# Performance work log

Measured on AMD Instinct MI355X. Metric: run time of the kernel, lower is better.

## Reference

```python
import jax, jax.numpy as jnp
import numpy as np

DIM = 1024
HEADS = 16


def setup_inputs() -> dict:
    key = jax.random.key(0)
    k1, k2, k3, k4 = jax.random.split(key, 4)
    x = jax.random.normal(k1, (2, 2048, DIM), dtype=jnp.float32)
    # nn.Linear(dim, dim*3, bias=False): weight [3*dim, dim], y = x @ W.T
    w_qkv = jax.random.normal(k2, (3 * DIM, DIM), dtype=jnp.float32) * (DIM ** -0.5)
    # nn.Linear(dim, dim) with bias
    w_out = jax.random.normal(k3, (DIM, DIM), dtype=jnp.float32) * (DIM ** -0.5)
    b_out = jax.random.normal(k4, (DIM,), dtype=jnp.float32) * 0.01
    return {"x": x, "w_qkv": w_qkv, "w_out": w_out, "b_out": b_out}


def reference(x, w_qkv, w_out, b_out):
    B, L, D = x.shape
    H = HEADS
    hd = D // H
    scale = D ** -0.5  # NOTE: module scales by full dim, not head_dim
    qkv = jnp.einsum('bld,ed->ble', x, w_qkv)          # [B, L, 3D]
    qkv = qkv.reshape(B, L, 3, H, hd)
    q = jnp.transpose(qkv[:, :, 0], (0, 2, 1, 3))       # [B, H, L, hd]
    k = jnp.transpose(qkv[:, :, 1], (0, 2, 1, 3))
    v = jnp.transpose(qkv[:, :, 2], (0, 2, 1, 3))
    attn = jnp.einsum('bhqd,bhkd->bhqk', q, k) * scale  # [B, H, L, L]
    attn = jax.nn.softmax(attn, axis=-1)
    o = jnp.einsum('bhqk,bhkd->bhqd', attn, v)           # [B, H, L, hd]
    o = jnp.transpose(o, (0, 2, 1, 3)).reshape(B, L, D)
    return jnp.einsum('bld,ed->ble', o, w_out) + b_out
```

## Files before the change

### kernel.cpp

```cpp
#include <hip/hip_runtime.h>


typedef __bf16 bf16;
typedef __bf16 bf16x4 __attribute__((ext_vector_type(4)));
typedef __bf16 bf16x8 __attribute__((ext_vector_type(8)));
typedef float  f32x4 __attribute__((ext_vector_type(4)));

#define MFMA32(A, B, C) __builtin_amdgcn_mfma_f32_16x16x32_bf16((A), (B), (C), 0, 0, 0)

static constexpr long QOFF  = 0;
static constexpr long KOFF  = 8388608;
static constexpr long VOFF  = 16777216;
static constexpr long FOFF  = 25165824;
static constexpr long WQOFF = 33554432;
static constexpr long WOOFF = 39845888;

#define QSCALE 0.045084222f

__device__ __forceinline__ void gl16(const bf16* g, bf16* l) {
  __builtin_amdgcn_global_load_lds((const __attribute__((address_space(1))) void*)g,
                                   (__attribute__((address_space(3))) void*)l, 16, 0, 0);
}

__device__ __forceinline__ f32x4 mfma16(bf16x4 a, bf16x4 b, f32x4 c) {
  asm("v_mfma_f32_16x16x16_bf16 %0, %1, %2, %0" : "+v"(c) : "v"(a), "v"(b));
  return c;
}

__device__ __forceinline__ float exp2fast(float x) {
#if __has_builtin(__builtin_amdgcn_exp2f)
  return __builtin_amdgcn_exp2f(x);
#else
  return exp2f(x);
#endif
}

__device__ __forceinline__ float max3f(float a, float b, float c) {
  return fmaxf(fmaxf(a, b), c);
}

__global__ __launch_bounds__(256)
void cvt_all(const float* __restrict__ x, const float* __restrict__ wq,
             const float* __restrict__ wo, bf16* __restrict__ xb,
             bf16* __restrict__ wqb, bf16* __restrict__ wob) {
  const int i = blockIdx.x * 256 + threadIdx.x;
  const float* in; bf16* out; long j;
  if (i < 524288)      { in = x;  out = xb;  j = i; }
  else if (i < 917504) { in = wq; out = wqb; j = i - 524288; }
  else                 { in = wo; out = wob; j = i - 917504; }
  const f32x4 v0 = *(const f32x4*)(in + j * 8);
  const f32x4 v1 = *(const f32x4*)(in + j * 8 + 4);
  bf16x8 o;
#pragma unroll
  for (int k = 0; k < 4; ++k) { o[k] = (bf16)v0[k]; o[k + 4] = (bf16)v1[k]; }
  *(bf16x8*)(out + j * 8) = o;
}

template <int MODE>
__global__ __launch_bounds__(256, 2)
void gemm_bt(const bf16* __restrict__ Ag, const bf16* __restrict__ Bg,
             float* __restrict__ outp, const float* __restrict__ bias,
             char* __restrict__ wsp)
{
  constexpr int K  = 1024;
  constexpr int NT = K / 32;
  const int bm = blockIdx.y, bn = blockIdx.x;
  const int tid  = threadIdx.x;
  const int lane = tid & 63;
  const int l15  = lane & 15, g = lane >> 4;
  const int wave = tid >> 6;
  const int wr = wave >> 1, wc = wave & 1;

  __shared__ __align__(16) bf16 Ab[2][128 * 40];
  __shared__ __align__(16) bf16 Bb[2][128 * 40];

  const int r  = tid >> 1;
  const int c0 = (tid & 1) * 16;

  const bf16* ap = Ag + (long)(bm * 128 + r) * K + c0;
  const bf16* bp = Bg + (long)(bn * 128 + r) * K + c0;

  bf16x8 a0, a1, b0, b1;
  f32x4 acc[4][4] = {};

  auto load_regs = [&](int t) {
    a0 = *(const bf16x8*)(ap + t * 32);
    a1 = *(const bf16x8*)(ap + t * 32 + 8);
    b0 = *(const bf16x8*)(bp + t * 32);
    b1 = *(const bf16x8*)(bp + t * 32 + 8);
  };
  auto store_lds = [&](int buf) {
    *(bf16x8*)&Ab[buf][r * 40 + c0]     = a0;
    *(bf16x8*)&Ab[buf][r * 40 + c0 + 8] = a1;
    *(bf16x8*)&Bb[buf][r * 40 + c0]     = b0;
    *(bf16x8*)&Bb[buf][r * 40 + c0 + 8] = b1;
  };

  load_regs(0);
  store_lds(0);
  __syncthreads();

#pragma unroll 2
  for (int t = 0; t < NT; ++t) {
    if (t + 1 < NT) load_regs(t + 1);
    const int buf = t & 1;
    bf16x8 af[4], bfv[4];
#pragma unroll
    for (int mf = 0; mf < 4; ++mf)
      af[mf] = *(const bf16x8*)&Ab[buf][(wr * 64 + mf * 16 + l15) * 40 + g * 8];
#pragma unroll
    for (int nf = 0; nf < 4; ++nf)
      bfv[nf] = *(const bf16x8*)&Bb[buf][(wc * 64 + nf * 16 + l15) * 40 + g * 8];
#pragma unroll
    for (int mf = 0; mf < 4; ++mf)
#pragma unroll
      for (int nf = 0; nf < 4; ++nf)
        acc[mf][nf] = MFMA32(af[mf], bfv[nf], acc[mf][nf]);
    if (t + 1 < NT) store_lds((t + 1) & 1);
    __syncthreads();
  }

  if constexpr (MODE == 0) {
    bf16* Qb = (bf16*)(wsp + QOFF);
    bf16* Kb = (bf16*)(wsp + KOFF);
    bf16* Vw = (bf16*)(wsp + VOFF);
#pragma unroll
    for (int nf = 0; nf < 4; ++nf) {
      const int colb = bn * 128 + wc * 64 + nf * 16 + l15;
      const int s = colb >> 10;
      const int h = (colb >> 6) & 15;
      const int d = colb & 63;
#pragma unroll
      for (int mf = 0; mf < 4; ++mf) {
#pragma unroll
        for (int rr = 0; rr < 4; ++rr) {
          const int rowg = bm * 128 + wr * 64 + mf * 16 + g * 4 + rr;
          const int bb = rowg >> 11, li = rowg & 2047;
          const float v = acc[mf][nf][rr];
          if (s == 0) {
            Qb[(long)((bb * 16 + h) * 2048 + li) * 64 + d] = (bf16)(v * QSCALE);
          } else if (s == 1) {
            const int sw = (((d >> 3) ^ (li & 7)) << 3) | (d & 7);
            Kb[(long)((bb * 16 + h) * 2048 + li) * 64 + sw] = (bf16)v;
          } else {
            const int lc = li & 63;
            const int sw = (((lc >> 3) ^ (d & 7)) << 3) | (lc & 7);
            Vw[(long)(bb * 16 + h) * 131072 + (li >> 6) * 4096 + d * 64 + sw] = (bf16)v;
          }
        }
      }
    }
  } else {
#pragma unroll
    for (int nf = 0; nf < 4; ++nf) {
      const int colg = bn * 128 + wc * 64 + nf * 16 + l15;
      const float bv = bias[colg];
#pragma unroll
      for (int mf = 0; mf < 4; ++mf) {
#pragma unroll
        for (int rr = 0; rr < 4; ++rr) {
          const int rowg = bm * 128 + wr * 64 + mf * 16 + g * 4 + rr;
          outp[(long)rowg * 1024 + colg] = acc[mf][nf][rr] + bv;
        }
      }
    }
  }
}

__global__ __launch_bounds__(256, 4)
void attn_fwd(const bf16* __restrict__ Q, const bf16* __restrict__ Kw,
              const bf16* __restrict__ Vw, bf16* __restrict__ Of)
{
  const int bid  = blockIdx.x;
  const int slot = bid >> 3;
  const int bh   = (bid & 7) * 4 + (slot >> 5);
  const int qt   = slot & 31;
  const int lane = threadIdx.x & 63;
  const int wave = threadIdx.x >> 6;
  const int l15  = lane & 15, g = lane >> 4;

  const bf16* Qh = Q  + (long)bh * 131072;
  const bf16* Ks = Kw + (long)bh * 131072;
  const bf16* Vs = Vw + (long)bh * 131072;

  __shared__ __align__(16) bf16 Klds[2][4096];
  __shared__ __align__(16) bf16 Vlds[2][4096];

  const int q0 = qt * 64 + wave * 16;

  bf16x8 qf[2];
#pragma unroll
  for (int ds = 0; ds < 2; ++ds)
    qf[ds] = *(const bf16x8*)(Qh + (q0 + l15) * 64 + ds * 32 + g * 8);

  auto stage = [&](int t, int buf) {
    const bf16* sk = Ks + t * 4096 + wave * 1024 + lane * 8;
    const bf16* sv = Vs + t * 4096 + wave * 1024 + lane * 8;
    gl16(sk,       &Klds[buf][wave * 1024]);
    gl16(sk + 512, &Klds[buf][wave * 1024 + 512]);
    gl16(sv,       &Vlds[buf][wave * 1024]);
    gl16(sv + 512, &Vlds[buf][wave * 1024 + 512]);
  };

  f32x4 o[4] = {};
  float m = -1e30f, ps = 0.f;

  stage(0, 0);
  __syncthreads();

  for (int t = 0; t < 32; ++t) {
    const int cur = t & 1;
    if (t < 31) stage(t + 1, cur ^ 1);

    f32x4 sf[4] = {};
#pragma unroll
    for (int kg = 0; kg < 4; ++kg)
#pragma unroll
      for (int ds = 0; ds < 2; ++ds) {
        const bf16x8 kf = *(const bf16x8*)
          &Klds[cur][(kg * 16 + l15) * 64 + (((ds * 4 + g) ^ (l15 & 7)) << 3)];
        sf[kg] = MFMA32(kf, qf[ds], sf[kg]);
      }

    const float t0 = max3f(sf[0][0], sf[0][1], sf[0][2]);
    const float t1 = max3f(sf[0][3], sf[1][0], sf[1][1]);
    const float t2 = max3f(sf[1][2], sf[1][3], sf[2][0]);
    const float t3 = max3f(sf[2][1], sf[2][2], sf[2][3]);
    const float t4 = max3f(sf[3][0], sf[3][1], sf[3][2]);
    float tm = fmaxf(max3f(t0, t1, t2), max3f(t3, t4, sf[3][3]));
    tm = fmaxf(tm, __shfl_xor(tm, 16));
    tm = fmaxf(tm, __shfl_xor(tm, 32));

    if (!__all(tm <= m + 8.f)) {
      const float nm = fmaxf(m, tm);
      const float al = exp2fast(m - nm);
      m = nm;
      ps *= al;
#pragma unroll
      for (int dg = 0; dg < 4; ++dg)
#pragma unroll
        for (int rr = 0; rr < 4; ++rr) o[dg][rr] *= al;
    }

    bf16x4 pa[4];
    float rs0 = 0.f, rs1 = 0.f, rs2 = 0.f, rs3 = 0.f;
#pragma unroll
    for (int kg = 0; kg < 4; ++kg) {
      const float p0 = exp2fast(sf[kg][0] - m);
      const float p1 = exp2fast(sf[kg][1] - m);
      const float p2 = exp2fast(sf[kg][2] - m);
      const float p3 = exp2fast(sf[kg][3] - m);
      rs0 += p0; rs1 += p1; rs2 += p2; rs3 += p3;
      pa[kg][0] = (bf16)p0; pa[kg][1] = (bf16)p1;
      pa[kg][2] = (bf16)p2; pa[kg][3] = (bf16)p3;
    }
    ps += (rs0 + rs1) + (rs2 + rs3);

#pragma unroll
    for (int kg = 0; kg < 4; ++kg)
#pragma unroll
      for (int dg = 0; dg < 4; ++dg) {
        const bf16x4 vb = *(const bf16x4*)
          &Vlds[cur][(dg * 16 + l15) * 64 +
                     (((2 * kg + (g >> 1)) ^ (l15 & 7)) << 3) + ((g & 1) << 2)];
        o[dg] = mfma16(vb, pa[kg], o[dg]);
      }
    __syncthreads();
  }

  ps += __shfl_xor(ps, 16);
  ps += __shfl_xor(ps, 32);
  const float inv = 1.f / ps;

  const int b = bh >> 4, h = bh & 15;
#pragma unroll
  for (int dg = 0; dg < 4; ++dg) {
    bf16x4 ov;
#pragma unroll
    for (int rr = 0; rr < 4; ++rr) ov[rr] = (bf16)(o[dg][rr] * inv);
    *(bf16x4*)(Of + (long)(b * 2048 + q0 + l15) * 1024 + h * 64 + dg * 16 + g * 4) = ov;
  }
}

extern "C" void kernel_launch(void* const* d_in, const int* in_sizes, int n_in,
                              void* d_out, int out_size, void* d_ws, size_t ws_size,
                              hipStream_t stream)
{
  (void)in_sizes; (void)n_in; (void)out_size; (void)ws_size;
  const float* x     = (const float*)d_in[0];
  const float* w_qkv = (const float*)d_in[1];
  const float* w_out = (const float*)d_in[2];
  const float* b_out = (const float*)d_in[3];
  float* out = (float*)d_out;
  char*  ws  = (char*)d_ws;

  bf16* Qb  = (bf16*)(ws + QOFF);
  bf16* Kb  = (bf16*)(ws + KOFF);
  bf16* Vw  = (bf16*)(ws + VOFF);
  bf16* xb  = (bf16*)(ws + FOFF);
  bf16* Ofb = (bf16*)(ws + FOFF);
  bf16* wqb = (bf16*)(ws + WQOFF);
  bf16* wob = (bf16*)(ws + WOOFF);

  cvt_all<<<dim3(4096), 256, 0, stream>>>(x, w_qkv, w_out, xb, wqb, wob);
  gemm_bt<0><<<dim3(24, 32), 256, 0, stream>>>(xb, wqb, nullptr, nullptr, ws);
  attn_fwd<<<dim3(1024), 256, 0, stream>>>(Qb, Kb, Vw, Ofb);
  gemm_bt<1><<<dim3(8, 32), 256, 0, stream>>>(Ofb, wob, out, b_out, ws);
}
```

Measured before the change: 135.7 us.

## Software-pipeline QK^T of next tile with softmax and PV of current tile

Restructures the flash-attention loop so the S=QK^T MFMAs for tile t+1 are issued before the softmax and PV work of tile t. K is prefetched two tiles ahead and V one tile ahead, using separate staging lambdas, and the loop is manually unrolled by two with ping-pong score registers. The goal is to overlap the exp/max VALU work with matrix-core work and hide LDS latency. In exchange it raises register pressure and adds more complex buffer-index logic, which must stay correct against the single per-iteration barrier.

```diff
diff --git a/kernel.cpp b/kernel.cpp
--- a/kernel.cpp
+++ b/kernel.cpp
@@ -193,80 +193,97 @@
   for (int ds = 0; ds < 2; ++ds)
     qf[ds] = *(const bf16x8*)(Qh + (q0 + l15) * 64 + ds * 32 + g * 8);
 
-  auto stage = [&](int t, int buf) {
+  auto stageK = [&](int t, int buf) {
     const bf16* sk = Ks + t * 4096 + wave * 1024 + lane * 8;
-    const bf16* sv = Vs + t * 4096 + wave * 1024 + lane * 8;
     gl16(sk,       &Klds[buf][wave * 1024]);
     gl16(sk + 512, &Klds[buf][wave * 1024 + 512]);
+  };
+  auto stageV = [&](int t, int buf) {
+    const bf16* sv = Vs + t * 4096 + wave * 1024 + lane * 8;
     gl16(sv,       &Vlds[buf][wave * 1024]);
     gl16(sv + 512, &Vlds[buf][wave * 1024 + 512]);
   };
 
   f32x4 o[4] = {};
   float m = -1e30f, ps = 0.f;
-
-  stage(0, 0);
+  f32x4 sfA[4], sfB[4];
+
+#define COMPUTE_S(BUF, SF) do {                                               \
+  _Pragma("unroll")                                                           \
+  for (int kg = 0; kg < 4; ++kg) {                                            \
+    SF[kg] = f32x4{0.f, 0.f, 0.f, 0.f};                                       \
+    _Pragma("unroll")                                                         \
+    for (int ds = 0; ds < 2; ++ds) {                                          \
+      const bf16x8 kf = *(const bf16x8*)                                      \
+        &Klds[BUF][(kg * 16 + l15) * 64 + (((ds * 4 + g) ^ (l15 & 7)) << 3)]; \
+      SF[kg] = MFMA32(kf, qf[ds], SF[kg]);                                    \
+    }                                                                         \
+  }                                                                           \
+} while (0)
+
+#define ATTN_BODY(T, SFC, SFN) do {                                           \
+  if ((T) <= 29) stageK((T) + 2, (T) & 1);                                    \
+  if ((T) <= 30) stageV((T) + 1, ((T) + 1) & 1);                              \
+  if ((T) <= 30) COMPUTE_S(((T) + 1) & 1, SFN);                               \
+  const float t0 = max3f(SFC[0][0], SFC[0][1], SFC[0][2]);                    \
+  const float t1 = max3f(SFC[0][3], SFC[1][0], SFC[1][1]);                    \
+  const float t2 = max3f(SFC[1][2], SFC[1][3], SFC[2][0]);                    \
+  const float t3 = max3f(SFC[2][1], SFC[2][2], SFC[2][3]);                    \
+  const float t4 = max3f(SFC[3][0], SFC[3][1], SFC[3][2]);                    \
+  float tm = fmaxf(max3f(t0, t1, t2), max3f(t3, t4, SFC[3][3]));              \
+  tm = fmaxf(tm, __shfl_xor(tm, 16));                                         \
+  tm = fmaxf(tm, __shfl_xor(tm, 32));                                         \
+  if (!__all(tm <= m + 8.f)) {                                                \
+    const float nm = fmaxf(m, tm);                                            \
+    const float al = exp2fast(m - nm);                                        \
+    m = nm;                                                                   \
+    ps *= al;                                                                 \
+    _Pragma("unroll")                                                         \
+    for (int dg = 0; dg < 4; ++dg)                                            \
+      _Pragma("unroll")                                                       \
+      for (int rr = 0; rr < 4; ++rr) o[dg][rr] *= al;                         \
+  }                                                                           \
+  bf16x4 pa[4];                                                               \
+  float rs0 = 0.f, rs1 = 0.f, rs2 = 0.f, rs3 = 0.f;                           \
+  _Pragma("unroll")                                                           \
+  for (int kg = 0; kg < 4; ++kg) {                                            \
+    const float p0 = exp2fast(SFC[kg][0] - m);                                \
+    const float p1 = exp2fast(SFC[kg][1] - m);                                \
+    const float p2 = exp2fast(SFC[kg][2] - m);                                \
+    const float p3 = exp2fast(SFC[kg][3] - m);                                \
+    rs0 += p0; rs1 += p1; rs2 += p2; rs3 += p3;                               \
+    pa[kg][0] = (bf16)p0; pa[kg][1] = (bf16)p1;                               \
+    pa[kg][2] = (bf16)p2; pa[kg][3] = (bf16)p3;                               \
+  }                                                                           \
+  ps += (rs0 + rs1) + (rs2 + rs3);                                            \
+  _Pragma("unroll")                                                           \
+  for (int kg = 0; kg < 4; ++kg)                                              \
+    _Pragma("unroll")                                                         \
+    for (int dg = 0; dg < 4; ++dg) {                                          \
+      const bf16x4 vb = *(const bf16x4*)                                      \
+        &Vlds[(T) & 1][(dg * 16 + l15) * 64 +                                 \
+                       (((2 * kg + (g >> 1)) ^ (l15 & 7)) << 3) +             \
+                       ((g & 1) << 2)];                                       \
+      o[dg] = mfma16(vb, pa[kg], o[dg]);                                      \
+    }                                                                         \
+  __syncthreads();                                                            \
+} while (0)
+
+  stageK(0, 0);
+  stageV(0, 0);
   __syncthreads();
-
-  for (int t = 0; t < 32; ++t) {
-    const int cur = t & 1;
-    if (t < 31) stage(t + 1, cur ^ 1);
-
-    f32x4 sf[4] = {};
-#pragma unroll
-    for (int kg = 0; kg < 4; ++kg)
-#pragma unroll
-      for (int ds = 0; ds < 2; ++ds) {
-        const bf16x8 kf = *(const bf16x8*)
-          &Klds[cur][(kg * 16 + l15) * 64 + (((ds * 4 + g) ^ (l15 & 7)) << 3)];
-        sf[kg] = MFMA32(kf, qf[ds], sf[kg]);
-      }
-
-    const float t0 = max3f(sf[0][0], sf[0][1], sf[0][2]);
-    const float t1 = max3f(sf[0][3], sf[1][0], sf[1][1]);
-    const float t2 = max3f(sf[1][2], sf[1][3], sf[2][0]);
-    const float t3 = max3f(sf[2][1], sf[2][2], sf[2][3]);
-    const float t4 = max3f(sf[3][0], sf[3][1], sf[3][2]);
-    float tm = fmaxf(max3f(t0, t1, t2), max3f(t3, t4, sf[3][3]));
-    tm = fmaxf(tm, __shfl_xor(tm, 16));
-    tm = fmaxf(tm, __shfl_xor(tm, 32));
-
-    if (!__all(tm <= m + 8.f)) {
-      const float nm = fmaxf(m, tm);
-      const float al = exp2fast(m - nm);
-      m = nm;
-      ps *= al;
-#pragma unroll
-      for (int dg = 0; dg < 4; ++dg)
-#pragma unroll
-        for (int rr = 0; rr < 4; ++rr) o[dg][rr] *= al;
-    }
-
-    bf16x4 pa[4];
-    float rs0 = 0.f, rs1 = 0.f, rs2 = 0.f, rs3 = 0.f;
-#pragma unroll
-    for (int kg = 0; kg < 4; ++kg) {
-      const float p0 = exp2fast(sf[kg][0] - m);
-      const float p1 = exp2fast(sf[kg][1] - m);
-      const float p2 = exp2fast(sf[kg][2] - m);
-      const float p3 = exp2fast(sf[kg][3] - m);
-      rs0 += p0; rs1 += p1; rs2 += p2; rs3 += p3;
-      pa[kg][0] = (bf16)p0; pa[kg][1] = (bf16)p1;
-      pa[kg][2] = (bf16)p2; pa[kg][3] = (bf16)p3;
-    }
-    ps += (rs0 + rs1) + (rs2 + rs3);
-
-#pragma unroll
-    for (int kg = 0; kg < 4; ++kg)
-#pragma unroll
-      for (int dg = 0; dg < 4; ++dg) {
-        const bf16x4 vb = *(const bf16x4*)
-          &Vlds[cur][(dg * 16 + l15) * 64 +
-                     (((2 * kg + (g >> 1)) ^ (l15 & 7)) << 3) + ((g & 1) << 2)];
-        o[dg] = mfma16(vb, pa[kg], o[dg]);
-      }
-    __syncthreads();
+  stageK(1, 1);
+  COMPUTE_S(0, sfA);
+  __syncthreads();
+
+#pragma unroll 1
+  for (int tp = 0; tp < 32; tp += 2) {
+    ATTN_BODY(tp, sfA, sfB);
+    ATTN_BODY(tp + 1, sfB, sfA);
   }
+
+#undef ATTN_BODY
+#undef COMPUTE_S
 
   ps += __shfl_xor(ps, 16);
   ps += __shfl_xor(ps, 32);
```

After: 135.3 us. Within noise of the previous version (-0.3%).
